# Kernel tuning notes

Measured on AMD Instinct MI355X. Metric: run time of the kernel, lower is better.

The kernel has to match this reference:

```python
import jax, jax.numpy as jnp
import numpy as np

NUM_POINTS = 72
GAMMA = 2.0
RADIUS = 15.0
W_CLS = 1.0
W_SIM = 3.0
LW_CLS = 2.0
LW_XYTL = 0.5
LW_LIOU = 2.0
K_MAX = 64
EPS = 1e-12  # F.normalize eps


def _normalize(v):
    # F.normalize over the flattened prior axis: v / max(||v||_2, eps)
    return v / jnp.maximum(jnp.linalg.norm(v), EPS)


def _liou_loss(pred, tgt):
    # pred: [..., P], tgt broadcastable; line IoU with radius, loss = 1 - iou
    lo = jnp.minimum(pred, tgt)
    hi = jnp.maximum(pred, tgt)
    ovr = (lo + RADIUS) - (hi - RADIUS)          # per-point overlap (may be < 0)
    union = (hi + RADIUS) - (lo - RADIUS)
    iou = jnp.sum(ovr, -1) / (jnp.sum(union, -1) + 1e-9)
    return 1.0 - iou


def _per_lane(feature, prior):
    # feature: [N, D] predictions for one image; prior: [D] one GT lane
    # ---- assignment cost ----
    logits = feature[:, :2]
    log_s = jax.nn.log_softmax(logits, axis=0)   # softmax over the N priors dim (dim=1 of [1,N,2])
    s = jnp.exp(log_s)
    focal_cost = jnp.sum(((1.0 - s) ** GAMMA) * log_s * prior[:2], axis=-1)  # [N]
    xy_cost = _normalize(jnp.sqrt(jnp.sum((feature[:, 3:5] - prior[3:5]) ** 2, -1)))  # [N]
    theta_cost = _normalize(feature[:, 5] - prior[5])                                  # [N]
    dis_cost = _normalize(jnp.sum(jnp.abs(feature[:, 6:] - prior[6:]), -1) / NUM_POINTS)  # [N]
    cost = W_SIM * (dis_cost * xy_cost * theta_cost) ** 2 + W_CLS * focal_cost
    # ---- dynamic top-k ----
    liou_all = _liou_loss(feature[:, 6:], prior[None, 6:])  # [N]
    k = jnp.clip(jnp.sum(liou_all).astype(jnp.int32), 1, K_MAX)
    _, idx = jax.lax.top_k(-cost, K_MAX)  # sorted ascending by cost; first k == topk(-cost, k)
    mask = (jnp.arange(K_MAX) < k).astype(feature.dtype)  # [K]
    kf = jnp.sum(mask)
    pf = feature[idx]  # [K, D] gathered predicted features
    # ---- xytl smooth-L1 on column-normalized concat([pred[:,2:6]; label[2:6]]) over valid rows ----
    rows = pf[:, 2:6]          # [K, 4]
    lab = prior[2:6]           # [4]
    colnorm = jnp.sqrt(jnp.sum((rows ** 2) * mask[:, None], 0) + lab ** 2)  # norm over the k+1 rows
    denom = jnp.maximum(colnorm, EPS)
    d = rows / denom - lab / denom  # [K, 4]
    ad = jnp.abs(d)
    sl1 = jnp.mean(jnp.where(ad < 1.0, 0.5 * d * d, ad - 0.5), -1)  # [K]
    sl1l = jnp.sum(sl1 * mask) / kf
    # ---- focal cls loss per assigned prior vs argmax of label cls ----
    tgt = jnp.argmax(prior[:2])
    lp = jax.nn.log_softmax(pf[:, :2], axis=-1)  # [K, 2]
    logpt = lp[:, tgt]
    pt = jnp.exp(logpt)
    fl_i = -((1.0 - pt) ** GAMMA) * logpt  # [K]
    fl = jnp.sum(fl_i * mask) / kf
    # ---- LIoU loss on assigned priors ----
    ll_i = _liou_loss(pf[:, 6:], prior[None, 6:])  # [K]
    ll = jnp.sum(ll_i * mask) / kf
    return sl1l, ll, fl


def setup_inputs() -> dict:
    key = jax.random.key(0)
    k1, k2 = jax.random.split(key)
    output = jax.random.normal(k1, (64, 1000, 78), dtype=jnp.float32)
    label = jax.random.normal(k2, (64, 16, 78), dtype=jnp.float32)
    return {"output": output, "label": label}


def reference(output, label):
    per_img = jax.vmap(_per_lane, in_axes=(None, 0))        # over lanes
    sl1l, ll, fl = jax.vmap(per_img, in_axes=(0, 0))(output, label)  # over batch
    sl1l = jnp.mean(sl1l)
    ll = jnp.mean(ll)
    fl = jnp.mean(fl)
    loss = (jnp.where(sl1l > 0, LW_XYTL * sl1l, 0.0)
            + jnp.where(ll > 0, LW_LIOU * ll, 0.0)
            + jnp.where(fl > 0, LW_CLS * fl, 0.0))
    return loss
```

## Files before the change

kernel.cpp:

```cpp
#include <hip/hip_runtime.h>
#include <math.h>

#define NROWS 1000
#define TWO_R_N 2160.0f
#define XSTRIDE 83
typedef unsigned int uint;
typedef unsigned long long ull;

__device__ __forceinline__ float wsumf(float v){
#pragma unroll
  for(int o=32;o;o>>=1) v += __shfl_xor(v,o,64);
  return v;
}
__device__ __forceinline__ float wmaxf(float v){
#pragma unroll
  for(int o=32;o;o>>=1) v = fmaxf(v,__shfl_xor(v,o,64));
  return v;
}

__global__ __launch_bounds__(256,2) void clr_task(const float* __restrict__ feat,
                                                  const float* __restrict__ lab,
                                                  float* __restrict__ ws)
{
  const int b  = blockIdx.x & 63;
  const int pg = blockIdx.x >> 6;
  const float* __restrict__ F  = feat + (size_t)b*NROWS*78;
  const float* __restrict__ PA = lab + ((size_t)b*16 + pg*2)*78;
  const float* __restrict__ PB = PA + 78;

  __shared__ float sX[4][16*XSTRIDE];
  __shared__ float sS [2][NROWS];
  __shared__ float sRT[2][NROWS];
  __shared__ float sC0[NROWS], sC1[NROWS];
  __shared__ float red[4][8];
  __shared__ int   selIdx[2][64];

  const int tid=threadIdx.x, wave=tid>>6, lane=tid&63;
  const int rloc16=lane>>2, q=lane&3;
  float* __restrict__ xp = &sX[wave][rloc16*XSTRIDE];

  float pva[18], pvb[18];
#pragma unroll
  for(int s=0;s<18;++s){ pva[s]=PA[6+q+4*s]; pvb[s]=PB[6+q+4*s]; }
  const float2* PA2=(const float2*)PA;
  const float2* PB2=(const float2*)PB;
  const float2 a01=PA2[0], a23=PA2[1], a45=PA2[2];
  const float2 b01=PB2[0], b23=PB2[1], b45=PB2[2];

  float accR0=0.f,accT0=0.f,accD0=0.f,accL0=0.f;
  float accR1=0.f,accT1=0.f,accD1=0.f,accL1=0.f;

#pragma unroll 2
  for(int pass=0; pass<16; ++pass){
    const int rr = pass*64 + wave*16 + rloc16;
    if(rr < NROWS){
      const float* __restrict__ rp = F + (size_t)rr*78;
      const float2 A0=*(const float2*)(rp+ 6+4*q), B0=*(const float2*)(rp+ 8+4*q);
      const float2 A1=*(const float2*)(rp+22+4*q), B1=*(const float2*)(rp+24+4*q);
      const float2 A2=*(const float2*)(rp+38+4*q), B2=*(const float2*)(rp+40+4*q);
      const float2 A3=*(const float2*)(rp+54+4*q), B3=*(const float2*)(rp+56+4*q);
      const float2 E =*(const float2*)(rp+70+2*q);
      xp[ 6+4*q]=A0.x; xp[ 7+4*q]=A0.y; xp[ 8+4*q]=B0.x; xp[ 9+4*q]=B0.y;
      xp[22+4*q]=A1.x; xp[23+4*q]=A1.y; xp[24+4*q]=B1.x; xp[25+4*q]=B1.y;
      xp[38+4*q]=A2.x; xp[39+4*q]=A2.y; xp[40+4*q]=B2.x; xp[41+4*q]=B2.y;
      xp[54+4*q]=A3.x; xp[55+4*q]=A3.y; xp[56+4*q]=B3.x; xp[57+4*q]=B3.y;
      xp[70+2*q]=E.x;  xp[71+2*q]=E.y;
      float part0=0.f, part1=0.f;
#pragma unroll
      for(int s=0;s<9;++s){
        const float x = xp[ 6+q+4*s];
        const float y = xp[42+q+4*s];
        part0 += fabsf(x - pva[s]);
        part0 += fabsf(y - pva[s+9]);
        part1 += fabsf(x - pvb[s]);
        part1 += fabsf(y - pvb[s+9]);
      }
      float s1a=part0+__shfl_xor(part0,1,64);
      float S0 = s1a +__shfl_xor(s1a, 2,64);
      float s1b=part1+__shfl_xor(part1,1,64);
      float S1 = s1b +__shfl_xor(s1b, 2,64);
      if(q==0){
        sS[0][rr]=S0; sS[1][rr]=S1;
        float d0=S0*(1.f/72.f); accD0+=d0*d0;
        accL0 += 1.f-(TWO_R_N-S0)/(TWO_R_N+S0+1e-9f);
        float d1=S1*(1.f/72.f); accD1+=d1*d1;
        accL1 += 1.f-(TWO_R_N-S1)/(TWO_R_N+S1+1e-9f);
      } else if(q==1){
        const float2* rp2=(const float2*)rp;
        const float2 c23=rp2[1], c45=rp2[2];
        float dr3=c23.y-a23.y, dr4=c45.x-a45.x, tt=c45.y-a45.y;
        float r2=dr3*dr3+dr4*dr4;
        sRT[0][rr]=sqrtf(r2)*tt; accR0+=r2; accT0+=tt*tt;
        dr3=c23.y-b23.y; dr4=c45.x-b45.x; tt=c45.y-b45.y;
        r2=dr3*dr3+dr4*dr4;
        sRT[1][rr]=sqrtf(r2)*tt; accR1+=r2; accT1+=tt*tt;
      } else if(q==2){
        const float2* rp2=(const float2*)rp;
        const float2 c01=rp2[0];
        sC0[rr]=c01.x; sC1[rr]=c01.y;
      }
    }
  }

  {
    float vR0=wsumf(accR0), vT0=wsumf(accT0), vD0=wsumf(accD0), vL0=wsumf(accL0);
    float vR1=wsumf(accR1), vT1=wsumf(accT1), vD1=wsumf(accD1), vL1=wsumf(accL1);
    if(lane==0){
      red[wave][0]=vR0; red[wave][1]=vT0; red[wave][2]=vD0; red[wave][3]=vL0;
      red[wave][4]=vR1; red[wave][5]=vT1; red[wave][6]=vD1; red[wave][7]=vL1;
    }
  }
  __syncthreads();
  if(wave>=2) return;
  const int w = wave;

  float R=0.f,T=0.f,D=0.f,L=0.f;
#pragma unroll
  for(int g=0;g<4;++g){
    R+=red[g][4*w]; T+=red[g][4*w+1]; D+=red[g][4*w+2]; L+=red[g][4*w+3];
  }
  float Nr=fmaxf(sqrtf(R),1e-12f), Nt=fmaxf(sqrtf(T),1e-12f), Nd=fmaxf(sqrtf(D),1e-12f);
  const float inv = 1.f/(Nr*Nt*Nd);
  int k=(int)L; if(k<1)k=1; if(k>64)k=64;

  float cx[16], cy[16], rt_[16], ssv[16];
#pragma unroll
  for(int t=0;t<16;++t){
    int i=t*64+lane; int ic=(i<NROWS)?i:(NROWS-1);
    cx[t]=sC0[ic]; cy[t]=sC1[ic]; rt_[t]=sRT[w][ic]; ssv[t]=sS[w][ic];
  }

  float m0=-INFINITY, m1=-INFINITY;
#pragma unroll
  for(int t=0;t<16;++t){ int i=t*64+lane; if(i<NROWS){ m0=fmaxf(m0,cx[t]); m1=fmaxf(m1,cy[t]); } }
  m0=wmaxf(m0); m1=wmaxf(m1);
  float s0=0.f, s1=0.f;
#pragma unroll
  for(int t=0;t<16;++t){ int i=t*64+lane; if(i<NROWS){ s0+=__expf(cx[t]-m0); s1+=__expf(cy[t]-m1); } }
  s0=wsumf(s0); s1=wsumf(s1);
  const float lse0=m0+__logf(s0), lse1=m1+__logf(s1);

  const float2 p01 = w ? b01 : a01;
  const float2 p23 = w ? b23 : a23;
  const float2 p45 = w ? b45 : a45;
  const float p0=p01.x, pp1=p01.y;

  uint key[16];
#pragma unroll
  for(int t=0;t<16;++t){
    int i=t*64+lane; uint kk=0xFFFFFFFFu;
    if(i<NROWS){
      float ls0=cx[t]-lse0, ls1=cy[t]-lse1;
      float e0=__expf(ls0), e1=__expf(ls1);
      float focal=(1.f-e0)*(1.f-e0)*ls0*p0 + (1.f-e1)*(1.f-e1)*ls1*pp1;
      float prod=rt_[t]*(ssv[t]*(1.f/72.f))*inv;
      float cost=3.f*prod*prod+focal;
      uint x=__float_as_uint(cost);
      kk=(x&0x80000000u)?~x:(x|0x80000000u);
    }
    key[t]=kk;
  }

  uint xx[16];
#pragma unroll
  for(int t=0;t<16;++t) xx[t]=key[t];
  uint pref=0u, r=(uint)k;
#pragma unroll
  for(int s=31;s>=0;--s){
    const uint bit=1u<<s;
    uint cnt=0u;
#pragma unroll
    for(int t=0;t<16;++t) cnt += (uint)__popcll(__ballot(xx[t]<bit));
    if(r>cnt){
      r-=cnt;
#pragma unroll
      for(int t=0;t<16;++t) xx[t]^=bit;
      pref|=bit;
    }
  }
  const uint T2=pref; uint need=r;

  const ull lmask=(1ull<<lane)-1ull;
  int base=0;
#pragma unroll
  for(int t=0;t<16;++t){
    bool lt = key[t]<T2;
    bool eq = key[t]==T2;
    ull meq=__ballot(eq);
    bool eqs = eq && ((uint)__popcll(meq&lmask)<need);
    uint teq=(uint)__popcll(meq);
    need -= (teq<need?teq:need);
    bool ssel = lt||eqs;
    ull ms=__ballot(ssel);
    if(ssel) selIdx[w][base+(int)__popcll(ms&lmask)] = t*64+lane;
    base += (int)__popcll(ms);
  }

  {
    bool act = lane<k;
    int idx = selIdx[w][act?lane:0];
    const float2* R2=(const float2*)(F+(size_t)idx*78);
    float2 g01=R2[0], g23=R2[1], g45=R2[2];
    float S = sS[w][idx];
    float mk = act?1.f:0.f;
    float n2=wsumf(g23.x*g23.x*mk), n3=wsumf(g23.y*g23.y*mk);
    float n4=wsumf(g45.x*g45.x*mk), n5=wsumf(g45.y*g45.y*mk);
    float l2=p23.x, l3=p23.y, l4=p45.x, l5=p45.y;
    float de2=fmaxf(sqrtf(n2+l2*l2),1e-12f);
    float de3=fmaxf(sqrtf(n3+l3*l3),1e-12f);
    float de4=fmaxf(sqrtf(n4+l4*l4),1e-12f);
    float de5=fmaxf(sqrtf(n5+l5*l5),1e-12f);
    float d2=g23.x/de2-l2/de2, d3=g23.y/de3-l3/de3, d4=g45.x/de4-l4/de4, d5=g45.y/de5-l5/de5;
    auto h=[](float d){ float ad=fabsf(d); return ad<1.f ? 0.5f*d*d : ad-0.5f; };
    float sl1 = 0.25f*(h(d2)+h(d3)+h(d4)+h(d5));
    float mm=fmaxf(g01.x,g01.y);
    float lsee=mm+__logf(__expf(g01.x-mm)+__expf(g01.y-mm));
    float logpt=((pp1>p0)?g01.y:g01.x)-lsee;
    float pt=__expf(logpt);
    float fl=-(1.f-pt)*(1.f-pt)*logpt;
    float ll=1.f-(TWO_R_N-S)/(TWO_R_N+S+1e-9f);
    float ssl=wsumf(sl1*mk), sll=wsumf(ll*mk), sfl=wsumf(fl*mk);
    if(lane==0){
      float invk=1.f/(float)k;
      float* o = ws + (size_t)(b*16 + pg*2 + w)*3;
      o[0]=ssl*invk; o[1]=sll*invk; o[2]=sfl*invk;
    }
  }
}

__global__ __launch_bounds__(256) void clr_finalize(const float* __restrict__ ws,
                                                    float* __restrict__ out)
{
  float a=0.f, bsum=0.f, c=0.f;
  for(int i=threadIdx.x;i<1024;i+=256){
    a    += ws[i*3+0];
    bsum += ws[i*3+1];
    c    += ws[i*3+2];
  }
  a=wsumf(a); bsum=wsumf(bsum); c=wsumf(c);
  __shared__ float r[12];
  int wave=threadIdx.x>>6, lane=threadIdx.x&63;
  if(lane==0){ r[wave*3]=a; r[wave*3+1]=bsum; r[wave*3+2]=c; }
  __syncthreads();
  if(threadIdx.x==0){
    float sa=0,sb=0,sc=0;
    for(int w2=0;w2<4;w2++){sa+=r[w2*3];sb+=r[w2*3+1];sc+=r[w2*3+2];}
    float sl1l=sa*(1.f/1024.f), ll=sb*(1.f/1024.f), fl=sc*(1.f/1024.f);
    float loss = (sl1l>0.f ? 0.5f*sl1l : 0.f)
               + (ll  >0.f ? 2.0f*ll   : 0.f)
               + (fl  >0.f ? 2.0f*fl   : 0.f);
    out[0]=loss;
  }
}

extern "C" void kernel_launch(void* const* d_in, const int* in_sizes, int n_in,
                              void* d_out, int out_size, void* d_ws, size_t ws_size,
                              hipStream_t stream)
{
  const float* feat = (const float*)d_in[0];
  const float* lab  = (const float*)d_in[1];
  float* ws  = (float*)d_ws;
  float* out = (float*)d_out;
  hipLaunchKernelGGL(clr_task, dim3(512), dim3(256), 0, stream, feat, lab, ws);
  hipLaunchKernelGGL(clr_finalize, dim3(1), dim3(256), 0, stream, ws, out);
}
```

Before: 98.80 us.

## Offload softmax LSE to idle waves and use 2-bit radix select steps

Waves 2 and 3 used to exit right after the reduction. They now compute the log-sum-exp of the two logit columns and pass it through shared memory, behind an extra barrier. The top-k threshold search now resolves two bits per step using three ballot counts, halving the serial dependent steps at the cost of more ballots overall. The selection compaction splits ballots and prefix counts into independent arrays to shorten the serial dependency chain; it also adds a redundant dummy shared write.

```diff
diff --git a/kernel.cpp b/kernel.cpp
--- a/kernel.cpp
+++ b/kernel.cpp
@@ -33,6 +33,7 @@
   __shared__ float sRT[2][NROWS];
   __shared__ float sC0[NROWS], sC1[NROWS];
   __shared__ float red[4][8];
+  __shared__ float sLse[2];
   __shared__ int   selIdx[2][64];
 
   const int tid=threadIdx.x, wave=tid>>6, lane=tid&63;
@@ -111,34 +112,39 @@
     }
   }
   __syncthreads();
+
+  float R=0.f,T=0.f,D=0.f,L=0.f;
+  float cx[16], cy[16], rt_[16], ssv[16];
+  const int w = wave;
+  if(wave>=2){
+    const float* __restrict__ col = (wave==2)? sC0 : sC1;
+    float m=-INFINITY;
+#pragma unroll
+    for(int t=0;t<16;++t){ int i=t*64+lane; if(i<NROWS) m=fmaxf(m,col[i]); }
+    m=wmaxf(m);
+    float ssum=0.f;
+#pragma unroll
+    for(int t=0;t<16;++t){ int i=t*64+lane; if(i<NROWS) ssum+=__expf(col[i]-m); }
+    ssum=wsumf(ssum);
+    if(lane==0) sLse[wave-2]=m+__logf(ssum);
+  } else {
+#pragma unroll
+    for(int g=0;g<4;++g){
+      R+=red[g][4*w]; T+=red[g][4*w+1]; D+=red[g][4*w+2]; L+=red[g][4*w+3];
+    }
+#pragma unroll
+    for(int t=0;t<16;++t){
+      int i=t*64+lane; int ic=(i<NROWS)?i:(NROWS-1);
+      cx[t]=sC0[ic]; cy[t]=sC1[ic]; rt_[t]=sRT[w][ic]; ssv[t]=sS[w][ic];
+    }
+  }
+  __syncthreads();
   if(wave>=2) return;
-  const int w = wave;
-
-  float R=0.f,T=0.f,D=0.f,L=0.f;
-#pragma unroll
-  for(int g=0;g<4;++g){
-    R+=red[g][4*w]; T+=red[g][4*w+1]; D+=red[g][4*w+2]; L+=red[g][4*w+3];
-  }
+
   float Nr=fmaxf(sqrtf(R),1e-12f), Nt=fmaxf(sqrtf(T),1e-12f), Nd=fmaxf(sqrtf(D),1e-12f);
   const float inv = 1.f/(Nr*Nt*Nd);
   int k=(int)L; if(k<1)k=1; if(k>64)k=64;
-
-  float cx[16], cy[16], rt_[16], ssv[16];
-#pragma unroll
-  for(int t=0;t<16;++t){
-    int i=t*64+lane; int ic=(i<NROWS)?i:(NROWS-1);
-    cx[t]=sC0[ic]; cy[t]=sC1[ic]; rt_[t]=sRT[w][ic]; ssv[t]=sS[w][ic];
-  }
-
-  float m0=-INFINITY, m1=-INFINITY;
-#pragma unroll
-  for(int t=0;t<16;++t){ int i=t*64+lane; if(i<NROWS){ m0=fmaxf(m0,cx[t]); m1=fmaxf(m1,cy[t]); } }
-  m0=wmaxf(m0); m1=wmaxf(m1);
-  float s0=0.f, s1=0.f;
-#pragma unroll
-  for(int t=0;t<16;++t){ int i=t*64+lane; if(i<NROWS){ s0+=__expf(cx[t]-m0); s1+=__expf(cy[t]-m1); } }
-  s0=wsumf(s0); s1=wsumf(s1);
-  const float lse0=m0+__logf(s0), lse1=m1+__logf(s1);
+  const float lse0=sLse[0], lse1=sLse[1];
 
   const float2 p01 = w ? b01 : a01;
   const float2 p23 = w ? b23 : a23;
@@ -166,34 +172,50 @@
   for(int t=0;t<16;++t) xx[t]=key[t];
   uint pref=0u, r=(uint)k;
 #pragma unroll
-  for(int s=31;s>=0;--s){
-    const uint bit=1u<<s;
-    uint cnt=0u;
-#pragma unroll
-    for(int t=0;t<16;++t) cnt += (uint)__popcll(__ballot(xx[t]<bit));
-    if(r>cnt){
-      r-=cnt;
-#pragma unroll
-      for(int t=0;t<16;++t) xx[t]^=bit;
-      pref|=bit;
-    }
-  }
-  const uint T2=pref; uint need=r;
+  for(int s=30;s>=0;s-=2){
+    const uint t1=1u<<s, t2=2u<<s, t3=3u<<s;
+    uint c1=0u,c2=0u,c3=0u;
+#pragma unroll
+    for(int t=0;t<16;++t){
+      uint v=xx[t];
+      c1+=(uint)__popcll(__ballot(v<t1));
+      c2+=(uint)__popcll(__ballot(v<t2));
+      c3+=(uint)__popcll(__ballot(v<t3));
+    }
+    uint bsel=(uint)(r>c1)+(uint)(r>c2)+(uint)(r>c3);
+    uint cb = bsel==0?0u:(bsel==1?c1:(bsel==2?c2:c3));
+    r -= cb;
+    const uint pb = bsel<<s;
+    pref |= pb;
+#pragma unroll
+    for(int t=0;t<16;++t) xx[t]^=pb;
+  }
+  const uint T2=pref;
 
   const ull lmask=(1ull<<lane)-1ull;
-  int base=0;
+  ull meq[16]; uint teq[16];
+#pragma unroll
+  for(int t=0;t<16;++t){ meq[t]=__ballot(key[t]==T2); teq[t]=(uint)__popcll(meq[t]); }
+  int cum=0; int nd[16];
+#pragma unroll
+  for(int t=0;t<16;++t){ nd[t]=(int)r-cum; cum+=(int)teq[t]; }
+  ull ms[16]; uint cnt_[16];
 #pragma unroll
   for(int t=0;t<16;++t){
-    bool lt = key[t]<T2;
     bool eq = key[t]==T2;
-    ull meq=__ballot(eq);
-    bool eqs = eq && ((uint)__popcll(meq&lmask)<need);
-    uint teq=(uint)__popcll(meq);
-    need -= (teq<need?teq:need);
-    bool ssel = lt||eqs;
-    ull ms=__ballot(ssel);
-    if(ssel) selIdx[w][base+(int)__popcll(ms&lmask)] = t*64+lane;
-    base += (int)__popcll(ms);
+    bool eqs = eq && ((int)__popcll(meq[t]&lmask) < nd[t]);
+    bool ssel = (key[t]<T2) || eqs;
+    ms[t]=__ballot(ssel); cnt_[t]=(uint)__popcll(ms[t]);
+    if(ssel) selIdx[w][0]=0;
+  }
+  int basev=0;
+#pragma unroll
+  for(int t=0;t<16;++t){
+    bool eq = key[t]==T2;
+    bool eqs = eq && ((int)__popcll(meq[t]&lmask) < nd[t]);
+    bool ssel = (key[t]<T2) || eqs;
+    if(ssel) selIdx[w][basev+(int)__popcll(ms[t]&lmask)] = t*64+lane;
+    basev += (int)cnt_[t];
   }
 
   {
```

New measurement: 100.0 us. No clear change (+1.3%).
